# Kernel optimization log

Hardware: AMD Instinct MI355X
Metric: run time of the kernel (lower is better)

Reference implementation:

```python
import jax, jax.numpy as jnp
import numpy as np

N = 50000   # nodes
E = 400000  # edges
D = 128     # hidden = out dim
H = 4       # heads
DH = 32     # head dim (D // H)
T = 3       # node types
R = 6       # relation (edge) types
L = 2       # layers
EPS = 1e-5


def setup_inputs() -> dict:
    key = jax.random.key(0)
    ks = jax.random.split(key, 12)
    s = D ** -0.5
    sh = DH ** -0.5
    return {
        "h": jax.random.normal(ks[0], (N, D), jnp.float32),
        "src": jax.random.randint(ks[1], (E,), 0, N),
        "dst": jax.random.randint(ks[2], (E,), 0, N),
        "ntype": jnp.sort(jax.random.randint(ks[3], (N,), 0, T)),
        "etype": jnp.sort(jax.random.randint(ks[4], (E,), 0, R)),
        # per-layer HGTConv params (stacked over L)
        "Wk": jax.random.normal(ks[5], (L, T, D, D), jnp.float32) * s,
        "Wq": jax.random.normal(ks[6], (L, T, D, D), jnp.float32) * s,
        "Wv": jax.random.normal(ks[7], (L, T, D, D), jnp.float32) * s,
        "Wa": jax.random.normal(ks[8], (L, T, D, D), jnp.float32) * s,
        "W_att": jax.random.normal(ks[9], (L, H, R, DH, DH), jnp.float32) * sh,
        "W_msg": jax.random.normal(ks[10], (L, H, R, DH, DH), jnp.float32) * sh,
        "pri": jnp.ones((L, H, R), jnp.float32),
        "skip": jnp.ones((L, T), jnp.float32),
        "ln_g": jnp.ones((L, D), jnp.float32),
        "ln_b": jnp.zeros((L, D), jnp.float32),
        # LayerAggregator params
        "agg_w": jnp.ones((L,), jnp.float32),
        "agg_g": jnp.ones((D,), jnp.float32),
        "agg_b": jnp.zeros((D,), jnp.float32),
    }


def typed_linear(x, types, W):
    # W: [T, in, out]; per-node-type linear (DGL TypedLinear, no bias)
    out = x @ W[0]
    for t in range(1, W.shape[0]):
        out = jnp.where((types == t)[:, None], x @ W[t], out)
    return out


def edge_typed(x, etype, W):
    # x: [E, H, DH]; W: [H, R, DH, DH]; per-relation, per-head linear
    out = jnp.einsum('ehd,hdo->eho', x, W[:, 0])
    for r in range(1, W.shape[1]):
        out = jnp.where((etype == r)[:, None, None],
                        jnp.einsum('ehd,hdo->eho', x, W[:, r]), out)
    return out


def layer_norm(x, g, b):
    mu = x.mean(-1, keepdims=True)
    var = ((x - mu) ** 2).mean(-1, keepdims=True)
    return (x - mu) * jax.lax.rsqrt(var + EPS) * g + b


def hgt_layer(x, src, dst, ntype, etype, Wk, Wq, Wv, Wa, W_att, W_msg, pri, skip):
    n = x.shape[0]
    k = typed_linear(x, ntype, Wk).reshape(n, H, DH)
    q = typed_linear(x, ntype, Wq).reshape(n, H, DH)
    v = typed_linear(x, ntype, Wv).reshape(n, H, DH)
    kw = edge_typed(k[src], etype, W_att)          # [E,H,DH]
    mv = edge_typed(v[src], etype, W_msg)          # [E,H,DH]
    a = (kw * q[dst]).sum(-1) * pri.T[etype] / np.sqrt(DH).astype(np.float32)  # [E,H]
    # edge softmax over destination nodes
    mx = jax.lax.stop_gradient(jax.ops.segment_max(a, dst, num_segments=n))
    ex = jnp.exp(a - mx[dst])
    den = jax.ops.segment_sum(ex, dst, num_segments=n)
    att = ex / den[dst]                             # [E,H]
    agg = jax.ops.segment_sum(att[:, :, None] * mv, dst, num_segments=n)
    h_a = typed_linear(agg.reshape(n, H * DH), ntype, Wa)
    sk = jax.nn.sigmoid(skip)[ntype][:, None]
    return h_a * sk + x * (1.0 - sk)                # skip gate (dropout = eval identity)


def reference(h, src, dst, ntype, etype, Wk, Wq, Wv, Wa, W_att, W_msg,
              pri, skip, ln_g, ln_b, agg_w, agg_g, agg_b):
    x = h
    outs = []
    for l in range(L):
        ho = hgt_layer(x, src, dst, ntype, etype, Wk[l], Wq[l], Wv[l], Wa[l],
                       W_att[l], W_msg[l], pri[l], skip[l])
        # residual is Identity (in_dim == out_dim), dropout is eval-mode identity
        x = layer_norm(x + ho, ln_g[l], ln_b[l])
        outs.append(x)
    w = jax.nn.softmax(agg_w)
    mixed = sum(w[i] * outs[i] for i in range(L))
    return layer_norm(mixed, agg_g, agg_b)  # [N, D]; per-type dict is just slicing by ntype
```

## Files before the change

### kernel.cpp

```cpp
#include <hip/hip_runtime.h>

#define NN 50000
#define NE 400000
#define DD 128
#define HH 4
#define DHH 32
#define TT 3
#define RR 6
#define LL 2
#define EPSF 1e-5f

typedef unsigned short ushort_t;
typedef unsigned int uint_t;
typedef __attribute__((ext_vector_type(8))) short short8_t;
typedef __attribute__((ext_vector_type(4))) float float4_t;

__device__ inline ushort_t f2bf(float f){
  union { float f; uint_t u; } x; x.f = f;
  uint_t r = x.u + 0x7fffu + ((x.u >> 16) & 1u);
  return (ushort_t)(r >> 16);
}
__device__ inline float bf2f(ushort_t u){
  union { uint_t u; float f; } x; x.u = ((uint_t)u) << 16;
  return x.f;
}
__device__ inline uint_t pack2(float a, float b){
  return (uint_t)f2bf(a) | ((uint_t)f2bf(b) << 16);
}

__global__ void hist_kernel(const int* __restrict__ dst, int* __restrict__ cnt){
  int e = blockIdx.x*256 + threadIdx.x;
  if (e < NE) atomicAdd(&cnt[dst[e]], 1);
}

__global__ void scan_kernel(const int* __restrict__ deg, int* __restrict__ rowptr){
  __shared__ int wsum[16];
  __shared__ int carrySh;
  int tid = threadIdx.x, lane = tid & 63, w = tid >> 6;
  if (tid == 0){ carrySh = 0; rowptr[0] = 0; }
  __syncthreads();
  for (int base = 0; base < NN; base += 1024){
    int i = base + tid;
    int v = (i < NN) ? deg[i] : 0;
    int s = v;
    #pragma unroll
    for (int off=1; off<64; off<<=1){ int t = __shfl_up(s, off); if (lane >= off) s += t; }
    if (lane == 63) wsum[w] = s;
    __syncthreads();
    if (w == 0 && lane < 16){
      int t = wsum[lane];
      #pragma unroll
      for (int off=1; off<16; off<<=1){ int u = __shfl_up(t, off); if (lane >= off) t += u; }
      wsum[lane] = t;
    }
    __syncthreads();
    int waveOff = (w == 0) ? 0 : wsum[w-1];
    int incl = s + waveOff + carrySh;
    if (i < NN) rowptr[i+1] = incl;
    __syncthreads();
    if (tid == 0) carrySh += wsum[15];
    __syncthreads();
  }
}

__global__ void scatter_kernel(const int* __restrict__ dst, const int* __restrict__ src,
                               const int* __restrict__ etype, const int* __restrict__ rowptr,
                               int* __restrict__ cnt, uint_t* __restrict__ sr, int* __restrict__ dp){
  int e = blockIdx.x*256 + threadIdx.x;
  if (e < NE){
    int d = dst[e];
    int pos = rowptr[d] + atomicAdd(&cnt[d], 1);
    sr[pos] = (uint_t)src[e] | ((uint_t)etype[e] << 27);
    dp[pos] = d;
  }
}

__global__ void wprep_kernel(const float* __restrict__ Wk, const float* __restrict__ Wq,
                             const float* __restrict__ Wv, const float* __restrict__ Wa,
                             ushort_t* __restrict__ Wkf, ushort_t* __restrict__ Wqf,
                             ushort_t* __restrict__ Wvf, ushort_t* __restrict__ Waf){
  int i = blockIdx.x*256 + threadIdx.x;
  if (i < TT*DD*DD){
    int j = i & 7, m = (i>>3)&15, kg = (i>>7)&3, ks = (i>>9)&3, tile = (i>>11)&7, t = i>>14;
    int d = ks*32 + kg*4 + (j&3) + ((j>>2)<<4);
    int o = tile*16 + m;
    size_t srcI = (size_t)t*16384 + (size_t)d*DD + o;
    Wkf[i] = f2bf(Wk[srcI]);
    Wqf[i] = f2bf(Wq[srcI]);
    Wvf[i] = f2bf(Wv[srcI]);
    Waf[i] = f2bf(Wa[srcI]);
  }
}

__global__ void wprep2_kernel(const float* __restrict__ Watt, const float* __restrict__ Wmsg,
                              ushort_t* __restrict__ Wattf, ushort_t* __restrict__ Wmsgf){
  int i = blockIdx.x*256 + threadIdx.x;
  if (i < HH*RR*DHH*DHH){
    int j = i & 7, m = (i>>3)&15, kg = (i>>7)&3;
    int tile = (i>>9) % 12, h = i / 6144;
    int nout = tile*16 + m;
    int r = nout >> 5, dd = nout & 31;
    int k = kg*4 + (j&3) + ((j>>2)<<4);
    Wattf[i] = f2bf(Watt[(((h*RR + r)*DHH + dd)<<5) + k]);
    Wmsgf[i] = f2bf(Wmsg[(((h*RR + r)*DHH + k)<<5) + dd]);
  }
}

__global__ __launch_bounds__(256) void kqv_kernel(
    const float* __restrict__ x, const int* __restrict__ ntype,
    const float* __restrict__ Wk, const float* __restrict__ Wq, const float* __restrict__ Wv,
    const ushort_t* __restrict__ Wkf, const ushort_t* __restrict__ Wqf, const ushort_t* __restrict__ Wvf,
    const ushort_t* __restrict__ Wattf, const ushort_t* __restrict__ Wmsgf,
    const float* __restrict__ pri,
    ushort_t* __restrict__ kout, ushort_t* __restrict__ qh, ushort_t* __restrict__ vhat)
{
  __shared__ int nts[16];
  __shared__ ushort_t smem[12352];
  ushort_t* xs_ = smem;
  ushort_t* qs_ = smem + 2112;
  ushort_t* vs_ = smem + 4224;
  ushort_t* ks_ = smem + 6336;
  ushort_t* stg = smem;
  int tid = threadIdx.x;
  int n0 = blockIdx.x * 16;
  if (tid < 16) nts[tid] = ntype[n0 + tid];
  #pragma unroll
  for (int it=0; it<8; it++){
    int i = tid + it*256;
    xs_[(i>>7)*132 + (i&127)] = f2bf(x[(size_t)n0*DD + i]);
  }
  __syncthreads();
  int t0 = nts[0];
  bool uni = true;
  #pragma unroll
  for (int j=1;j<16;j++) uni = uni && (nts[j] == t0);

  int lane = tid & 63;
  union U8 { struct { uint2 lo, hi; } u; short8_t s; uint4 q; };

  if (uni){
    int w = tid >> 6;
    int m = lane & 15, kg = lane >> 4;
    float4_t acck0{0.f,0.f,0.f,0.f}, acck1{0.f,0.f,0.f,0.f};
    float4_t accq0{0.f,0.f,0.f,0.f}, accq1{0.f,0.f,0.f,0.f};
    float4_t accv0{0.f,0.f,0.f,0.f}, accv1{0.f,0.f,0.f,0.f};
    const ushort_t* wkf = Wkf + (size_t)t0*16384;
    const ushort_t* wqf = Wqf + (size_t)t0*16384;
    const ushort_t* wvf = Wvf + (size_t)t0*16384;
    int tA = 2*w, tB = 2*w+1;
    #pragma unroll
    for (int ks=0; ks<4; ks++){
      U8 a_;
      a_.u.lo = *(const uint2*)&xs_[m*132 + ks*32 + kg*4];
      a_.u.hi = *(const uint2*)&xs_[m*132 + ks*32 + kg*4 + 16];
      int offA = (((tA*4 + ks)*4 + kg) << 7) + (m << 3);
      int offB = (((tB*4 + ks)*4 + kg) << 7) + (m << 3);
      U8 bk0, bk1, bq0, bq1, bv0, bv1;
      bk0.q = *(const uint4*)(wkf + offA);
      bk1.q = *(const uint4*)(wkf + offB);
      bq0.q = *(const uint4*)(wqf + offA);
      bq1.q = *(const uint4*)(wqf + offB);
      bv0.q = *(const uint4*)(wvf + offA);
      bv1.q = *(const uint4*)(wvf + offB);
      acck0 = __builtin_amdgcn_mfma_f32_16x16x32_bf16(bk0.s, a_.s, acck0, 0,0,0);
      acck1 = __builtin_amdgcn_mfma_f32_16x16x32_bf16(bk1.s, a_.s, acck1, 0,0,0);
      accq0 = __builtin_amdgcn_mfma_f32_16x16x32_bf16(bq0.s, a_.s, accq0, 0,0,0);
      accq1 = __builtin_amdgcn_mfma_f32_16x16x32_bf16(bq1.s, a_.s, accq1, 0,0,0);
      accv0 = __builtin_amdgcn_mfma_f32_16x16x32_bf16(bv0.s, a_.s, accv0, 0,0,0);
      accv1 = __builtin_amdgcn_mfma_f32_16x16x32_bf16(bv1.s, a_.s, accv1, 0,0,0);
    }
    int cA = tA*16 + (kg<<2), cB = tB*16 + (kg<<2);
    *(uint2*)(&ks_[m*132 + cA]) = make_uint2(pack2(acck0[0],acck0[1]), pack2(acck0[2],acck0[3]));
    *(uint2*)(&ks_[m*132 + cB]) = make_uint2(pack2(acck1[0],acck1[1]), pack2(acck1[2],acck1[3]));
    *(uint2*)(&qs_[m*132 + cA]) = make_uint2(pack2(accq0[0],accq0[1]), pack2(accq0[2],accq0[3]));
    *(uint2*)(&qs_[m*132 + cB]) = make_uint2(pack2(accq1[0],accq1[1]), pack2(accq1[2],accq1[3]));
    *(uint2*)(&vs_[m*132 + cA]) = make_uint2(pack2(accv0[0],accv0[1]), pack2(accv0[2],accv0[3]));
    *(uint2*)(&vs_[m*132 + cB]) = make_uint2(pack2(accv1[0],accv1[1]), pack2(accv1[2],accv1[3]));
  } else {
    int c = tid & 127, nb = (tid >> 7) * 8;
    float ak[8], aq[8], av[8];
    #pragma unroll
    for (int j=0;j<8;j++){ ak[j]=0.f; aq[j]=0.f; av[j]=0.f; }
    #pragma unroll
    for (int j=0;j<8;j++){
      int t = nts[nb+j];
      const float* wk = Wk + (size_t)t*DD*DD + c;
      const float* wq = Wq + (size_t)t*DD*DD + c;
      const float* wv = Wv + (size_t)t*DD*DD + c;
      float sk=0.f, sq=0.f, sv=0.f;
      for (int d=0; d<DD; d++){
        float xv = bf2f(xs_[(nb+j)*132 + d]);
        sk += xv*wk[d*DD];
        sq += xv*wq[d*DD];
        sv += xv*wv[d*DD];
      }
      ak[j]=sk; aq[j]=sq; av[j]=sv;
    }
    #pragma unroll
    for (int j=0;j<8;j++){
      ks_[(nb+j)*132 + c]=f2bf(ak[j]);
      qs_[(nb+j)*132 + c]=f2bf(aq[j]);
      vs_[(nb+j)*132 + c]=f2bf(av[j]);
    }
  }
  __syncthreads();

  int h = tid >> 6;
  int m = lane & 15, kg = lane >> 4;
  U8 aq_, av_;
  aq_.u.lo = *(const uint2*)&qs_[m*132 + (h<<5) + (kg<<2)];
  aq_.u.hi = *(const uint2*)&qs_[m*132 + (h<<5) + (kg<<2) + 16];
  av_.u.lo = *(const uint2*)&vs_[m*132 + (h<<5) + (kg<<2)];
  av_.u.hi = *(const uint2*)&vs_[m*132 + (h<<5) + (kg<<2) + 16];
  {
    int row = tid >> 4, coff = (tid & 15) * 8;
    uint4 kv4;
    kv4.x = *(const uint_t*)&ks_[row*132 + coff];
    kv4.y = *(const uint_t*)&ks_[row*132 + coff + 2];
    kv4.z = *(const uint_t*)&ks_[row*132 + coff + 4];
    kv4.w = *(const uint_t*)&ks_[row*132 + coff + 6];
    *(uint4*)(kout + (size_t)(n0+row)*DD + coff) = kv4;
  }
  __syncthreads();

  const ushort_t* wqb = Wattf + h*(RR*DHH*DHH);
  const ushort_t* wvb = Wmsgf + h*(RR*DHH*DHH);

  #pragma unroll
  for (int nt=0; nt<12; nt++){
    int frag = ((nt*4 + kg)<<7) + (m<<3);
    U8 bq_;
    bq_.q = *(const uint4*)(wqb + frag);
    float4_t accq{0.f,0.f,0.f,0.f};
    accq = __builtin_amdgcn_mfma_f32_16x16x32_bf16(bq_.s, aq_.s, accq, 0,0,0);
    int nout0 = nt*16 + (kg<<2);
    int r = nout0 >> 5, dd0 = nout0 & 31;
    float scale = pri[h*RR + r] * 0.17677669529663687f;
    *(uint2*)(&stg[m*772 + r*DD + (h<<5) + dd0]) =
        make_uint2(pack2(accq[0]*scale, accq[1]*scale), pack2(accq[2]*scale, accq[3]*scale));
  }
  __syncthreads();
  #pragma unroll
  for (int it=0; it<6; it++){
    int idx = tid + it*256;
    int row = idx / 96;
    int off = (idx - row*96) * 8;
    uint4 q4;
    q4.x = *(const uint_t*)&stg[row*772 + off];
    q4.y = *(const uint_t*)&stg[row*772 + off + 2];
    q4.z = *(const uint_t*)&stg[row*772 + off + 4];
    q4.w = *(const uint_t*)&stg[row*772 + off + 6];
    *(uint4*)(qh + (size_t)(n0+row)*768 + off) = q4;
  }
  __syncthreads();

  #pragma unroll
  for (int nt=0; nt<12; nt++){
    int frag = ((nt*4 + kg)<<7) + (m<<3);
    U8 bv_;
    bv_.q = *(const uint4*)(wvb + frag);
    float4_t accv{0.f,0.f,0.f,0.f};
    accv = __builtin_amdgcn_mfma_f32_16x16x32_bf16(bv_.s, av_.s, accv, 0,0,0);
    int nout0 = nt*16 + (kg<<2);
    int r = nout0 >> 5, dd0 = nout0 & 31;
    *(uint2*)(&stg[m*772 + r*DD + (h<<5) + dd0]) =
        make_uint2(pack2(accv[0],accv[1]), pack2(accv[2],accv[3]));
  }
  __syncthreads();
  #pragma unroll
  for (int it=0; it<6; it++){
    int idx = tid + it*256;
    int row = idx / 96;
    int off = (idx - row*96) * 8;
    uint4 v4;
    v4.x = *(const uint_t*)&stg[row*772 + off];
    v4.y = *(const uint_t*)&stg[row*772 + off + 2];
    v4.z = *(const uint_t*)&stg[row*772 + off + 4];
    v4.w = *(const uint_t*)&stg[row*772 + off + 6];
    *(uint4*)(vhat + (size_t)(n0+row)*768 + off) = v4;
  }
}

__global__ __launch_bounds__(256) void logit_kernel(
    const ushort_t* __restrict__ kb, const ushort_t* __restrict__ qh,
    const uint_t* __restrict__ src_r, const int* __restrict__ dstp,
    float* __restrict__ aout)
{
  int idx = blockIdx.x*256 + threadIdx.x;
  int p = idx >> 2;
  if (p >= NE) return;
  int h = idx & 3;
  uint_t sr = src_r[p];
  int s = (int)(sr & 0x07FFFFFFu);
  int r = (int)(sr >> 27);
  int dn = dstp[p];
  const uint_t* kr = (const uint_t*)(kb + (size_t)s*DD + (h<<5));
  const uint_t* qr = (const uint_t*)(qh + ((size_t)dn*RR + r)*DD + (h<<5));
  float a = 0.f;
  #pragma unroll
  for (int i4=0; i4<4; i4++){
    uint4 kw = ((const uint4*)kr)[i4];
    uint4 qw = ((const uint4*)qr)[i4];
    a += bf2f((ushort_t)(kw.x&0xffffu))*bf2f((ushort_t)(qw.x&0xffffu))
       + bf2f((ushort_t)(kw.x>>16))   *bf2f((ushort_t)(qw.x>>16))
       + bf2f((ushort_t)(kw.y&0xffffu))*bf2f((ushort_t)(qw.y&0xffffu))
       + bf2f((ushort_t)(kw.y>>16))   *bf2f((ushort_t)(qw.y>>16))
       + bf2f((ushort_t)(kw.z&0xffffu))*bf2f((ushort_t)(qw.z&0xffffu))
       + bf2f((ushort_t)(kw.z>>16))   *bf2f((ushort_t)(qw.z>>16))
       + bf2f((ushort_t)(kw.w&0xffffu))*bf2f((ushort_t)(qw.w&0xffffu))
       + bf2f((ushort_t)(kw.w>>16))   *bf2f((ushort_t)(qw.w>>16));
  }
  aout[(size_t)p*HH + h] = a;
}

__global__ __launch_bounds__(256) void reduce_kernel(
    const ushort_t* __restrict__ vhat, const float* __restrict__ aout,
    const int* __restrict__ rowptr, const uint_t* __restrict__ src_r,
    ushort_t* __restrict__ agg16)
{
  int n = blockIdx.x*4 + (threadIdx.x >> 6);
  if (n >= NN) return;
  int lane = threadIdx.x & 63;
  int h = lane >> 4;
  int b = rowptr[n], e1 = rowptr[n+1];
  float m = -1e30f;
  for (int i=b;i<e1;i++) m = fmaxf(m, aout[(size_t)i*HH + h]);
  float den = 0.f, ac0 = 0.f, ac1 = 0.f;
  for (int i=b; i<e1; i+=8){
    int m8 = e1 - i; if (m8 > 8) m8 = 8;
    uint_t sr8[8]; float a8[8];
    #pragma unroll
    for (int jj=0;jj<8;jj++){
      int idx2 = i + ((jj < m8) ? jj : (m8-1));
      sr8[jj] = src_r[idx2];
      a8[jj] = (jj < m8) ? aout[(size_t)idx2*HH + h] : -1e30f;
    }
    uint_t vv8[8];
    #pragma unroll
    for (int jj=0;jj<8;jj++){
      uint_t sr_ = sr8[jj];
      vv8[jj] = *(const uint_t*)(vhat + ((size_t)(sr_ & 0x07FFFFFFu)*RR + (sr_>>27))*DD + (lane<<1));
    }
    #pragma unroll
    for (int jj=0;jj<8;jj++){
      float ex = __expf(a8[jj] - m);
      den += ex;
      ac0 += ex * bf2f((ushort_t)(vv8[jj] & 0xffffu));
      ac1 += ex * bf2f((ushort_t)(vv8[jj] >> 16));
    }
  }
  float inv = (den > 0.f) ? 1.f/den : 0.f;
  uint_t packed = (uint_t)f2bf(ac0*inv) | ((uint_t)f2bf(ac1*inv) << 16);
  *(uint_t*)(agg16 + (size_t)n*DD + (lane<<1)) = packed;
}

__global__ __launch_bounds__(256) void ha_kernel(
    const ushort_t* __restrict__ agg16, const float* __restrict__ x, const int* __restrict__ ntype,
    const float* __restrict__ Wa, const ushort_t* __restrict__ Waf, const float* __restrict__ skipl,
    const float* __restrict__ lng, const float* __restrict__ lnb,
    float* __restrict__ xout)
{
  __shared__ ushort_t as[16][132];
  __shared__ float xs[16][132];
  __shared__ int nts[16];
  int tid = threadIdx.x;
  int n0 = blockIdx.x * 16;
  {
    int row = tid >> 4, col = (tid & 15) * 8;
    uint4 t4 = *(const uint4*)(agg16 + (size_t)(n0+row)*DD + col);
    *(uint2*)&as[row][col]   = make_uint2(t4.x, t4.y);
    *(uint2*)&as[row][col+4] = make_uint2(t4.z, t4.w);
  }
  if (tid < 16) nts[tid] = ntype[n0 + tid];
  __syncthreads();
  int t0 = nts[0];
  bool uni = true;
  #pragma unroll
  for (int j=1;j<16;j++) uni = uni && (nts[j] == t0);

  if (uni){
    int lane = tid & 63, w = tid >> 6;
    int m = lane & 15, kg = lane >> 4;
    float4_t acc0{0.f,0.f,0.f,0.f}, acc1{0.f,0.f,0.f,0.f};
    const ushort_t* waf = Waf + (size_t)t0*16384;
    int tA = 2*w, tB = 2*w+1;
    union U8 { struct { uint2 lo, hi; } u; short8_t s; uint4 q; };
    #pragma unroll
    for (int ks=0; ks<4; ks++){
      U8 a_;
      a_.u.lo = *(const uint2*)&as[m][ks*32 + kg*4];
      a_.u.hi = *(const uint2*)&as[m][ks*32 + kg*4 + 16];
      U8 b0, b1;
      b0.q = *(const uint4*)(waf + ((((tA*4 + ks)*4 + kg) << 7) + (m << 3)));
      b1.q = *(const uint4*)(waf + ((((tB*4 + ks)*4 + kg) << 7) + (m << 3)));
      acc0 = __builtin_amdgcn_mfma_f32_16x16x32_bf16(b0.s, a_.s, acc0, 0,0,0);
      acc1 = __builtin_amdgcn_mfma_f32_16x16x32_bf16(b1.s, a_.s, acc1, 0,0,0);
    }
    float sk = 1.f/(1.f + __expf(-skipl[t0]));
    int cA = tA*16 + (kg<<2), cB = tB*16 + (kg<<2);
    #pragma unroll
    for (int i=0;i<4;i++){
      float xva = x[(size_t)(n0+m)*DD + cA + i];
      float xvb = x[(size_t)(n0+m)*DD + cB + i];
      xs[m][cA+i] = acc0[i]*sk + xva*(2.f - sk);
      xs[m][cB+i] = acc1[i]*sk + xvb*(2.f - sk);
    }
  } else {
    int c = tid & 127, nb = (tid >> 7) * 8;
    float acc[8];
    #pragma unroll
    for (int j=0;j<8;j++) acc[j]=0.f;
    #pragma unroll
    for (int j=0;j<8;j++){
      int t = nts[nb+j];
      const float* wa = Wa + (size_t)t*DD*DD + c;
      float sacc2 = 0.f;
      for (int d=0; d<DD; d++)
        sacc2 += bf2f(as[nb+j][d]) * wa[d*DD];
      acc[j] = sacc2;
    }
    #pragma unroll
    for (int j=0;j<8;j++){
      int n = n0 + nb + j;
      float sk2 = 1.f/(1.f + __expf(-skipl[nts[nb+j]]));
      float xv = x[(size_t)n*DD + c];
      xs[nb+j][c] = acc[j]*sk2 + xv*(2.f - sk2);
    }
  }
  __syncthreads();
  int lane = tid & 63;
  int r0 = tid >> 6;
  #pragma unroll
  for (int rr = r0; rr < 16; rr += 4){
    float t0v = xs[rr][lane], t1v = xs[rr][lane+64];
    float s = t0v + t1v;
    #pragma unroll
    for (int off=32; off>0; off>>=1) s += __shfl_xor(s, off);
    float mu = s * (1.f/DD);
    float d0 = t0v-mu, d1 = t1v-mu;
    float vs = d0*d0 + d1*d1;
    #pragma unroll
    for (int off=32; off>0; off>>=1) vs += __shfl_xor(vs, off);
    float inv = rsqrtf(vs*(1.f/DD) + EPSF);
    size_t base = (size_t)(n0+rr)*DD;
    xout[base+lane]    = d0*inv*lng[lane]    + lnb[lane];
    xout[base+lane+64] = d1*inv*lng[lane+64] + lnb[lane+64];
  }
}

__global__ __launch_bounds__(256) void final_kernel(
    const float* __restrict__ x1, const float* __restrict__ x2,
    const float* __restrict__ aggw, const float* __restrict__ g, const float* __restrict__ b,
    float* __restrict__ out)
{
  int lane = threadIdx.x & 63;
  int n = blockIdx.x*4 + (threadIdx.x >> 6);
  float a0 = aggw[0], a1 = aggw[1];
  float m = fmaxf(a0, a1);
  float e0 = __expf(a0-m), e1 = __expf(a1-m);
  float inv01 = 1.f/(e0+e1);
  float w0 = e0*inv01, w1 = e1*inv01;
  size_t base = (size_t)n*DD;
  float t0 = w0*x1[base+lane]    + w1*x2[base+lane];
  float t1 = w0*x1[base+lane+64] + w1*x2[base+lane+64];
  float s = t0 + t1;
  #pragma unroll
  for (int off=32; off>0; off>>=1) s += __shfl_xor(s, off);
  float mu = s * (1.f/DD);
  float d0 = t0-mu, d1 = t1-mu;
  float vs = d0*d0 + d1*d1;
  #pragma unroll
  for (int off=32; off>0; off>>=1) vs += __shfl_xor(vs, off);
  float invv = rsqrtf(vs*(1.f/DD) + EPSF);
  out[base+lane]    = d0*invv*g[lane]    + b[lane];
  out[base+lane+64] = d1*invv*g[lane+64] + b[lane+64];
}

extern "C" void kernel_launch(void* const* d_in, const int* in_sizes, int n_in,
                              void* d_out, int out_size, void* d_ws, size_t ws_size,
                              hipStream_t stream)
{
  (void)in_sizes; (void)n_in; (void)out_size; (void)ws_size;
  const float* h_in  = (const float*)d_in[0];
  const int*   src   = (const int*)d_in[1];
  const int*   dst   = (const int*)d_in[2];
  const int*   ntype = (const int*)d_in[3];
  const int*   etype = (const int*)d_in[4];
  const float* Wk    = (const float*)d_in[5];
  const float* Wq    = (const float*)d_in[6];
  const float* Wv    = (const float*)d_in[7];
  const float* Wa    = (const float*)d_in[8];
  const float* Watt  = (const float*)d_in[9];
  const float* Wmsg  = (const float*)d_in[10];
  const float* pri   = (const float*)d_in[11];
  const float* skp   = (const float*)d_in[12];
  const float* lng   = (const float*)d_in[13];
  const float* lnb   = (const float*)d_in[14];
  const float* aggw  = (const float*)d_in[15];
  const float* aggg  = (const float*)d_in[16];
  const float* aggb_ = (const float*)d_in[17];

  size_t P = (size_t)NN*DD;
  ushort_t* kb16 = (ushort_t*)d_ws;
  ushort_t* qh   = kb16 + P;
  ushort_t* vhat = qh + (size_t)NN*RR*DD;
  float* aoutb = (float*)(vhat + (size_t)NN*RR*DD);
  float* out0  = aoutb + (size_t)NE*HH;
  int* rowptr = (int*)(out0 + P);
  int* cnt    = rowptr + NN + 1;
  uint_t* srcr = (uint_t*)(cnt + NN);
  int* dstp   = (int*)(srcr + NE);
  ushort_t* wkF = (ushort_t*)(dstp + NE);
  ushort_t* wqF = wkF + (size_t)TT*DD*DD;
  ushort_t* wvF = wqF + (size_t)TT*DD*DD;
  ushort_t* waF = wvF + (size_t)TT*DD*DD;
  ushort_t* wattF = waF + (size_t)TT*DD*DD;
  ushort_t* wmsgF = wattF + (size_t)HH*RR*DHH*DHH;
  ushort_t* agg16 = qh;
  float* xout = (float*)d_out;

  hipMemsetAsync(cnt, 0, NN*sizeof(int), stream);
  hist_kernel<<<(NE+255)/256, 256, 0, stream>>>(dst, cnt);
  scan_kernel<<<1, 1024, 0, stream>>>(cnt, rowptr);
  hipMemsetAsync(cnt, 0, NN*sizeof(int), stream);
  scatter_kernel<<<(NE+255)/256, 256, 0, stream>>>(dst, src, etype, rowptr, cnt, srcr, dstp);

  const float* x = h_in;
  for (int l=0; l<LL; l++){
    const float* Wk_l  = Wk  + (size_t)l*TT*DD*DD;
    const float* Wq_l  = Wq  + (size_t)l*TT*DD*DD;
    const float* Wv_l  = Wv  + (size_t)l*TT*DD*DD;
    const float* Wa_l  = Wa  + (size_t)l*TT*DD*DD;
    const float* Wat_l = Watt + (size_t)l*HH*RR*DHH*DHH;
    const float* Wms_l = Wmsg + (size_t)l*HH*RR*DHH*DHH;
    const float* pri_l = pri + (size_t)l*HH*RR;
    const float* skp_l = skp + (size_t)l*TT;

    wprep_kernel<<<(TT*DD*DD+255)/256, 256, 0, stream>>>(Wk_l, Wq_l, Wv_l, Wa_l,
                                                         wkF, wqF, wvF, waF);
    wprep2_kernel<<<(HH*RR*DHH*DHH+255)/256, 256, 0, stream>>>(Wat_l, Wms_l, wattF, wmsgF);
    kqv_kernel<<<NN/16, 256, 0, stream>>>(x, ntype, Wk_l, Wq_l, Wv_l, wkF, wqF, wvF,
                                          wattF, wmsgF, pri_l, kb16, qh, vhat);
    logit_kernel<<<(NE*HH+255)/256, 256, 0, stream>>>(kb16, qh, srcr, dstp, aoutb);
    reduce_kernel<<<(NN+3)/4, 256, 0, stream>>>(vhat, aoutb, rowptr, srcr, agg16);
    float* xo = (l == 0) ? out0 : xout;
    ha_kernel<<<NN/16, 256, 0, stream>>>(agg16, x, ntype, Wa_l, waF, skp_l,
                                         lng + (size_t)l*DD, lnb + (size_t)l*DD, xo);
    x = xo;
  }
  final_kernel<<<NN/4, 256, 0, stream>>>(out0, xout, aggw, aggg, aggb_, xout);
}
```

Before: 455.6 us.

## Double-buffer q/v staging in kqv kernel and use nontemporal global stores

Adds a second LDS staging buffer so the v-projection MFMA results can be written while the q staging buffer is still being copied out, which removes one __syncthreads between the q store loop and the v compute. The k, qh and vhat global writes now use nontemporal stores to avoid polluting cache with large streamed outputs. Doubling shared memory per block (about 49KB) may reduce occupancy, and nontemporal stores could hurt if the later logit and aggregation kernels would have hit these lines in cache.

```diff
diff --git a/kernel.cpp b/kernel.cpp
--- a/kernel.cpp
+++ b/kernel.cpp
@@ -14,6 +14,7 @@
 typedef unsigned int uint_t;
 typedef __attribute__((ext_vector_type(8))) short short8_t;
 typedef __attribute__((ext_vector_type(4))) float float4_t;
+typedef __attribute__((ext_vector_type(4))) uint_t uint4v;
 
 __device__ inline ushort_t f2bf(float f){
   union { float f; uint_t u; } x; x.f = f;
@@ -115,12 +116,13 @@
     ushort_t* __restrict__ kout, ushort_t* __restrict__ qh, ushort_t* __restrict__ vhat)
 {
   __shared__ int nts[16];
-  __shared__ ushort_t smem[12352];
+  __shared__ ushort_t smem[24704];
   ushort_t* xs_ = smem;
   ushort_t* qs_ = smem + 2112;
   ushort_t* vs_ = smem + 4224;
   ushort_t* ks_ = smem + 6336;
-  ushort_t* stg = smem;
+  ushort_t* stg1 = smem;
+  ushort_t* stg2 = smem + 12352;
   int tid = threadIdx.x;
   int n0 = blockIdx.x * 16;
   if (tid < 16) nts[tid] = ntype[n0 + tid];
@@ -214,12 +216,12 @@
   av_.u.hi = *(const uint2*)&vs_[m*132 + (h<<5) + (kg<<2) + 16];
   {
     int row = tid >> 4, coff = (tid & 15) * 8;
-    uint4 kv4;
+    uint4v kv4;
     kv4.x = *(const uint_t*)&ks_[row*132 + coff];
     kv4.y = *(const uint_t*)&ks_[row*132 + coff + 2];
     kv4.z = *(const uint_t*)&ks_[row*132 + coff + 4];
     kv4.w = *(const uint_t*)&ks_[row*132 + coff + 6];
-    *(uint4*)(kout + (size_t)(n0+row)*DD + coff) = kv4;
+    __builtin_nontemporal_store(kv4, (uint4v*)(kout + (size_t)(n0+row)*DD + coff));
   }
   __syncthreads();
 
@@ -236,24 +238,23 @@
     int nout0 = nt*16 + (kg<<2);
     int r = nout0 >> 5, dd0 = nout0 & 31;
     float scale = pri[h*RR + r] * 0.17677669529663687f;
-    *(uint2*)(&stg[m*772 + r*DD + (h<<5) + dd0]) =
+    *(uint2*)(&stg1[m*772 + r*DD + (h<<5) + dd0]) =
         make_uint2(pack2(accq[0]*scale, accq[1]*scale), pack2(accq[2]*scale, accq[3]*scale));
   }
   __syncthreads();
+
   #pragma unroll
   for (int it=0; it<6; it++){
     int idx = tid + it*256;
     int row = idx / 96;
     int off = (idx - row*96) * 8;
-    uint4 q4;
-    q4.x = *(const uint_t*)&stg[row*772 + off];
-    q4.y = *(const uint_t*)&stg[row*772 + off + 2];
-    q4.z = *(const uint_t*)&stg[row*772 + off + 4];
-    q4.w = *(const uint_t*)&stg[row*772 + off + 6];
-    *(uint4*)(qh + (size_t)(n0+row)*768 + off) = q4;
-  }
-  __syncthreads();
-
+    uint4v q4;
+    q4.x = *(const uint_t*)&stg1[row*772 + off];
+    q4.y = *(const uint_t*)&stg1[row*772 + off + 2];
+    q4.z = *(const uint_t*)&stg1[row*772 + off + 4];
+    q4.w = *(const uint_t*)&stg1[row*772 + off + 6];
+    __builtin_nontemporal_store(q4, (uint4v*)(qh + (size_t)(n0+row)*768 + off));
+  }
   #pragma unroll
   for (int nt=0; nt<12; nt++){
     int frag = ((nt*4 + kg)<<7) + (m<<3);
@@ -263,21 +264,22 @@
     accv = __builtin_amdgcn_mfma_f32_16x16x32_bf16(bv_.s, av_.s, accv, 0,0,0);
     int nout0 = nt*16 + (kg<<2);
     int r = nout0 >> 5, dd0 = nout0 & 31;
-    *(uint2*)(&stg[m*772 + r*DD + (h<<5) + dd0]) =
+    *(uint2*)(&stg2[m*772 + r*DD + (h<<5) + dd0]) =
         make_uint2(pack2(accv[0],accv[1]), pack2(accv[2],accv[3]));
   }
   __syncthreads();
+
   #pragma unroll
   for (int it=0; it<6; it++){
     int idx = tid + it*256;
     int row = idx / 96;
     int off = (idx - row*96) * 8;
-    uint4 v4;
-    v4.x = *(const uint_t*)&stg[row*772 + off];
-    v4.y = *(const uint_t*)&stg[row*772 + off + 2];
-    v4.z = *(const uint_t*)&stg[row*772 + off + 4];
-    v4.w = *(const uint_t*)&stg[row*772 + off + 6];
-    *(uint4*)(vhat + (size_t)(n0+row)*768 + off) = v4;
+    uint4v v4;
+    v4.x = *(const uint_t*)&stg2[row*772 + off];
+    v4.y = *(const uint_t*)&stg2[row*772 + off + 2];
+    v4.z = *(const uint_t*)&stg2[row*772 + off + 4];
+    v4.w = *(const uint_t*)&stg2[row*772 + off + 6];
+    __builtin_nontemporal_store(v4, (uint4v*)(vhat + (size_t)(n0+row)*768 + off));
   }
 }
 
```

Measured after the change: 473.0 us. 1.04x slower.
